# Kernel tuning notes

Hardware: AMD Instinct MI355X
Metric: run time of the kernel (lower is better)

The kernel has to match this reference:

```python
import jax, jax.numpy as jnp
import numpy as np

N = 50000      # nodes
E = 1600000    # edges
IN_DIM = 128
HID = 32
OUT = 32
HEADS = 4
NEG_SLOPE = 0.2  # DGL GATConv default leaky_relu slope


def setup_inputs() -> dict:
    key = jax.random.key(0)
    ks = jax.random.split(key, 16)
    h = jax.random.normal(ks[0], (N, IN_DIM), dtype=jnp.float32)
    src = jax.random.randint(ks[1], (E,), 0, N, dtype=jnp.int32)
    dst = jax.random.randint(ks[2], (E,), 0, N, dtype=jnp.int32)
    s = 0.1
    # layer 1: in_dim -> (HEADS, HID)
    W1 = jax.random.normal(ks[3], (IN_DIM, HEADS * HID), dtype=jnp.float32) * s
    al1 = jax.random.normal(ks[4], (HEADS, HID), dtype=jnp.float32) * s
    ar1 = jax.random.normal(ks[5], (HEADS, HID), dtype=jnp.float32) * s
    b1 = jnp.zeros((HEADS * HID,), dtype=jnp.float32)
    # layer 2: HEADS*HID -> (HEADS, HID)
    W2 = jax.random.normal(ks[6], (HEADS * HID, HEADS * HID), dtype=jnp.float32) * s
    al2 = jax.random.normal(ks[7], (HEADS, HID), dtype=jnp.float32) * s
    ar2 = jax.random.normal(ks[8], (HEADS, HID), dtype=jnp.float32) * s
    b2 = jnp.zeros((HEADS * HID,), dtype=jnp.float32)
    # layer 3: HEADS*HID -> (HEADS, OUT)
    W3 = jax.random.normal(ks[9], (HEADS * HID, HEADS * OUT), dtype=jnp.float32) * s
    al3 = jax.random.normal(ks[10], (HEADS, OUT), dtype=jnp.float32) * s
    ar3 = jax.random.normal(ks[11], (HEADS, OUT), dtype=jnp.float32) * s
    b3 = jnp.zeros((HEADS * OUT,), dtype=jnp.float32)
    return {"h": h, "src": src, "dst": dst,
            "W1": W1, "al1": al1, "ar1": ar1, "b1": b1,
            "W2": W2, "al2": al2, "ar2": ar2, "b2": b2,
            "W3": W3, "al3": al3, "ar3": ar3, "b3": b3}


def gat_layer(h, W, al, ar, b, src, dst):
    """DGL-style GATConv. h:[N,F] -> [N,H,D]."""
    H, D = al.shape
    ft = (h @ W).reshape(-1, H, D)                      # [N,H,D]
    el = jnp.einsum('nhd,hd->nh', ft, al)               # [N,H]
    er = jnp.einsum('nhd,hd->nh', ft, ar)               # [N,H]
    e = jax.nn.leaky_relu(el[src] + er[dst], NEG_SLOPE)  # [E,H]
    # edge softmax grouped by destination node
    m = jax.ops.segment_max(e, dst, num_segments=N)     # [N,H]
    ex = jnp.exp(e - m[dst])
    z = jax.ops.segment_sum(ex, dst, num_segments=N)    # [N,H]
    a = ex / z[dst]                                     # [E,H]
    msg = ft[src] * a[:, :, None]                       # [E,H,D]
    rst = jax.ops.segment_sum(msg, dst, num_segments=N)  # [N,H,D]
    return rst + b.reshape(1, H, D)


def reference(h, src, dst, W1, al1, ar1, b1, W2, al2, ar2, b2, W3, al3, ar3, b3):
    x = gat_layer(h, W1, al1, ar1, b1, src, dst).reshape(N, -1)  # flatten(1)
    x = jax.nn.elu(x)  # dropout is identity at eval
    x = gat_layer(x, W2, al2, ar2, b2, src, dst).reshape(N, -1)
    x = jax.nn.elu(x)
    x = gat_layer(x, W3, al3, ar3, b3, src, dst).mean(axis=1)    # [N,OUT]
    return x
```

## Files before the change

### kernel.cpp

```cpp
#include <hip/hip_runtime.h>
#include <hip/hip_fp16.h>

#define NEG_SLOPE 0.2f
#define LOG2E 1.44269504088896340736f
#define C1   2048
#define BKT  196
#define BSTR 9216

typedef _Float16 half8 __attribute__((ext_vector_type(8)));
typedef float    f32x4 __attribute__((ext_vector_type(4)));

__device__ __forceinline__ unsigned int encf(float f) {
    unsigned int u = __float_as_uint(f);
    return (u & 0x80000000u) ? ~u : (u | 0x80000000u);
}
__device__ __forceinline__ float decf(unsigned int u) {
    return (u & 0x80000000u) ? __uint_as_float(u & 0x7fffffffu)
                             : __uint_as_float(~u);
}

__global__ __launch_bounds__(256) void wprep(const float* __restrict__ W1,
    const float* __restrict__ W2, const float* __restrict__ W3,
    __half* __restrict__ Wt)
{
    __shared__ float tile[32][33];
    const int b = blockIdx.x;
    const float* W = (b < 16) ? W1 : (b < 32) ? W2 : W3;
    __half* out = Wt + (size_t)(b >> 4) * (128 * 128);
    const int tb = b & 15;
    const int k0 = (tb >> 2) * 32;
    const int c0 = (tb & 3) * 32;
    const int t = threadIdx.x;
    const int tx = t & 31, ty = t >> 5;
#pragma unroll
    for (int p = 0; p < 4; ++p)
        tile[p * 8 + ty][tx] = W[(size_t)(k0 + p * 8 + ty) * 128 + c0 + tx];
    __syncthreads();
#pragma unroll
    for (int p = 0; p < 4; ++p) {
        const int c = c0 + p * 8 + ty;
        out[(size_t)c * 128 + k0 + tx] = __float2half(tile[tx][p * 8 + ty]);
    }
}

__global__ __launch_bounds__(256) void gemm_mfma(const float* __restrict__ X,
    const __half* __restrict__ Wt, const float* __restrict__ al,
    const float* __restrict__ ar, __half* __restrict__ C16,
    float* __restrict__ el, float* __restrict__ er,
    unsigned int* __restrict__ maxbuf, int M)
{
    __shared__ __align__(16) char Xs[64 * 256];
    __shared__ __align__(16) char Ws[128 * 256];
    __shared__ unsigned int lmax[8];
    const int t = threadIdx.x;
    const int l = t & 63;
    const int w = t >> 6;
    const int row0 = blockIdx.x * 64;
    if (t < 8) lmax[t] = 0;

    {
        const int r = t >> 2;
        int gr = row0 + r; if (gr >= M) gr = M - 1;
        const float4* s4 = (const float4*)&X[(size_t)gr * 128 + (t & 3) * 32];
        const unsigned swz = ((unsigned)(r & 7)) << 4;
        char* base = Xs + r * 256;
#pragma unroll
        for (int u = 0; u < 4; ++u) {
            float4 a = s4[2 * u], b = s4[2 * u + 1];
            half8 hv;
            hv[0] = (_Float16)a.x; hv[1] = (_Float16)a.y;
            hv[2] = (_Float16)a.z; hv[3] = (_Float16)a.w;
            hv[4] = (_Float16)b.x; hv[5] = (_Float16)b.y;
            hv[6] = (_Float16)b.z; hv[7] = (_Float16)b.w;
            *(half8*)(base + (((t & 3) * 64 + u * 16) ^ swz)) = hv;
        }
    }
    {
        const int c = t >> 1;
        const char* src = (const char*)Wt + (size_t)c * 256 + (t & 1) * 128;
        const unsigned swz = ((unsigned)(c & 7)) << 4;
        char* base = Ws + c * 256;
#pragma unroll
        for (int u = 0; u < 8; ++u) {
            uint4 v = *(const uint4*)(src + u * 16);
            *(uint4*)(base + (((t & 1) * 128 + u * 16) ^ swz)) = v;
        }
    }
    __syncthreads();

    const int wr = w * 16;
    const int rA = l & 15;
    const int kq = l >> 4;

    half8 af[4];
    {
        const int row = wr + rA;
        const unsigned swz = ((unsigned)(row & 7)) << 4;
        const char* base = Xs + row * 256;
#pragma unroll
        for (int kk = 0; kk < 4; ++kk)
            af[kk] = *(const half8*)(base + (((unsigned)(kk * 64 + kq * 16)) ^ swz));
    }
    f32x4 acc[8];
#pragma unroll
    for (int ct = 0; ct < 8; ++ct) { acc[ct][0]=0.f; acc[ct][1]=0.f; acc[ct][2]=0.f; acc[ct][3]=0.f; }
#pragma unroll
    for (int ct = 0; ct < 8; ++ct) {
        const int c = ct * 16 + rA;
        const unsigned swz = ((unsigned)(c & 7)) << 4;
        const char* base = Ws + c * 256;
#pragma unroll
        for (int kk = 0; kk < 4; ++kk) {
            half8 bf = *(const half8*)(base + (((unsigned)(kk * 64 + kq * 16)) ^ swz));
            acc[ct] = __builtin_amdgcn_mfma_f32_16x16x32_f16(af[kk], bf, acc[ct], 0, 0, 0);
        }
    }

    float pl[4][4], pr[4][4];
#pragma unroll
    for (int h = 0; h < 4; ++h)
#pragma unroll
        for (int r = 0; r < 4; ++r) { pl[h][r] = 0.f; pr[h][r] = 0.f; }
#pragma unroll
    for (int ct = 0; ct < 8; ++ct) {
        const int col = ct * 16 + rA;
        const float av = al[col] * LOG2E;
        const float rv = ar[col] * LOG2E;
        const int h = ct >> 1;
#pragma unroll
        for (int r = 0; r < 4; ++r) {
            pl[h][r] += acc[ct][r] * av;
            pr[h][r] += acc[ct][r] * rv;
        }
    }
#pragma unroll
    for (int off = 1; off < 16; off <<= 1) {
#pragma unroll
        for (int h = 0; h < 4; ++h)
#pragma unroll
            for (int r = 0; r < 4; ++r) {
                pl[h][r] += __shfl_xor(pl[h][r], off);
                pr[h][r] += __shfl_xor(pr[h][r], off);
            }
    }
    if (rA == 0) {
#pragma unroll
        for (int r = 0; r < 4; ++r) {
            const int gr = row0 + wr + kq * 4 + r;
            if (gr < M) {
                *(float4*)&el[(size_t)gr * 4] =
                    make_float4(pl[0][r], pl[1][r], pl[2][r], pl[3][r]);
                *(float4*)&er[(size_t)gr * 4] =
                    make_float4(pr[0][r], pr[1][r], pr[2][r], pr[3][r]);
            }
        }
#pragma unroll
        for (int h = 0; h < 4; ++h) {
            float ml = fmaxf(fmaxf(pl[h][0], pl[h][1]), fmaxf(pl[h][2], pl[h][3]));
            float mr = fmaxf(fmaxf(pr[h][0], pr[h][1]), fmaxf(pr[h][2], pr[h][3]));
            atomicMax(&lmax[h], encf(ml));
            atomicMax(&lmax[4 + h], encf(mr));
        }
    }

    {
        char* slice = Xs + wr * 256;
#pragma unroll
        for (int ct = 0; ct < 8; ++ct) {
            const int colb = (ct * 16 + rA) * 2;
#pragma unroll
            for (int r = 0; r < 4; ++r) {
                const int rowL = kq * 4 + r;
                const unsigned swz = ((unsigned)(rowL & 7)) << 4;
                *(__half*)(slice + rowL * 256 + ((unsigned)colb ^ swz)) =
                    __float2half(acc[ct][r]);
            }
        }
        const int rowL = l >> 2;
        const unsigned swz = ((unsigned)(rowL & 7)) << 4;
        const int gr = row0 + wr + rowL;
#pragma unroll
        for (int u = 0; u < 4; ++u) {
            const unsigned bo = (unsigned)((l & 3) * 64 + u * 16);
            uint4 v = *(const uint4*)(slice + rowL * 256 + (bo ^ swz));
            if (gr < M) *(uint4*)&C16[(size_t)gr * 128 + bo / 2] = v;
        }
    }
    __syncthreads();
    if (t < 8) atomicMax(&maxbuf[t], lmax[t]);
}

__global__ __launch_bounds__(256) void p1_bucket(const int* __restrict__ src,
    const int* __restrict__ dst, unsigned int* __restrict__ tmp,
    unsigned int* __restrict__ bcnt, int E_)
{
    __shared__ unsigned int hist[256];
    __shared__ unsigned int sc[256];
    __shared__ unsigned int ebase[256];
    __shared__ unsigned int gbase[256];
    __shared__ unsigned int buf[C1];
    __shared__ unsigned int off[C1];
    const int t  = threadIdx.x;
    const int e0 = blockIdx.x * C1;
    hist[t] = 0;
    __syncthreads();
    int  s_[8], d_[8];
    bool v_[8];
#pragma unroll
    for (int k = 0; k < 2; ++k) {
        int idx = e0 + k * 1024 + t * 4;
        if (idx + 3 < E_) {
            int4 sv = *(const int4*)&src[idx];
            int4 dv = *(const int4*)&dst[idx];
            s_[k*4+0]=sv.x; s_[k*4+1]=sv.y; s_[k*4+2]=sv.z; s_[k*4+3]=sv.w;
            d_[k*4+0]=dv.x; d_[k*4+1]=dv.y; d_[k*4+2]=dv.z; d_[k*4+3]=dv.w;
            v_[k*4+0]=true; v_[k*4+1]=true; v_[k*4+2]=true; v_[k*4+3]=true;
        } else {
            for (int j = 0; j < 4; ++j) {
                int e = idx + j;
                v_[k*4+j] = e < E_;
                s_[k*4+j] = v_[k*4+j] ? src[e] : 0;
                d_[k*4+j] = v_[k*4+j] ? dst[e] : 0;
            }
        }
    }
#pragma unroll
    for (int j = 0; j < 8; ++j) if (v_[j]) atomicAdd(&hist[d_[j] >> 8], 1u);
    __syncthreads();
    const unsigned int cnt_t = hist[t];
    sc[t] = cnt_t;
    __syncthreads();
    for (int o = 1; o < 256; o <<= 1) {
        unsigned int v = (t >= o) ? sc[t - o] : 0;
        __syncthreads();
        sc[t] += v;
        __syncthreads();
    }
    const unsigned int excl = sc[t] - cnt_t;
    ebase[t] = excl;
    gbase[t] = (t < BKT && cnt_t > 0) ? atomicAdd(&bcnt[t], cnt_t) : 0u;
    hist[t] = excl;
    __syncthreads();
#pragma unroll
    for (int j = 0; j < 8; ++j) {
        if (v_[j]) {
            const int b = d_[j] >> 8;
            unsigned int pos  = atomicAdd(&hist[b], 1u);
            unsigned int go   = gbase[b] + (pos - ebase[b]);
            buf[pos] = ((unsigned int)s_[j] << 8) | (unsigned int)(d_[j] & 255);
            off[pos] = (go < BSTR) ? ((unsigned int)b * BSTR + go) : 0xFFFFFFFFu;
        }
    }
    __syncthreads();
    const int total = min(C1, E_ - e0);
    for (int i = t; i < total; i += 256) {
        unsigned int u = off[i];
        if (u != 0xFFFFFFFFu) tmp[u] = buf[i];
    }
}

__global__ __launch_bounds__(256) void scanB(const unsigned int* __restrict__ bcnt,
    unsigned int* __restrict__ bbase, unsigned int* __restrict__ maxinit, int E_)
{
    __shared__ unsigned int sc[256];
    const int t = threadIdx.x;
    const unsigned int v = (t < BKT) ? bcnt[t] : 0;
    sc[t] = v;
    __syncthreads();
    for (int off = 1; off < 256; off <<= 1) {
        unsigned int u = (t >= off) ? sc[t - off] : 0;
        __syncthreads();
        sc[t] += u;
        __syncthreads();
    }
    if (t < BKT) bbase[t] = sc[t] - v;
    if (t == BKT) bbase[t] = (unsigned int)E_;
    if (t < 24) maxinit[t] = 0;
}

__global__ __launch_bounds__(512) void p2_scatter(const unsigned int* __restrict__ tmp,
    const unsigned int* __restrict__ bcnt, const unsigned int* __restrict__ bbase,
    int* __restrict__ rowptr, int* __restrict__ esrc_s, int Nn)
{
    __shared__ unsigned int hist[256], sc[256], cur[256];
    __shared__ unsigned int ent[BSTR];
    const int t = threadIdx.x;
    const int b = blockIdx.x;
    const unsigned int cnt  = min(bcnt[b], (unsigned int)BSTR);
    const unsigned int base = bbase[b];
    if (t < 256) hist[t] = 0;
    __syncthreads();
    for (unsigned int i = t; i < cnt; i += 512) {
        unsigned int e = tmp[(size_t)b * BSTR + i];
        ent[i] = e;
        atomicAdd(&hist[e & 255u], 1u);
    }
    __syncthreads();
    unsigned int c_t = 0;
    if (t < 256) { c_t = hist[t]; sc[t] = c_t; }
    __syncthreads();
    for (int off = 1; off < 256; off <<= 1) {
        unsigned int u = (t < 256 && t >= off) ? sc[t - off] : 0;
        __syncthreads();
        if (t < 256) sc[t] += u;
        __syncthreads();
    }
    if (t < 256) {
        const unsigned int excl = sc[t] - c_t;
        cur[t] = base + excl;
        const int n = (b << 8) + t;
        if (n <= Nn) rowptr[n] = (int)(base + excl);
    }
    __syncthreads();
    for (unsigned int i = t; i < cnt; i += 512) {
        unsigned int e = ent[i];
        unsigned int p = atomicAdd(&cur[e & 255u], 1u);
        esrc_s[p] = (int)(e >> 8);
    }
}

template <int MODE>
__global__ __launch_bounds__(256) void attn_agg(
    const __half* __restrict__ ft, const float* __restrict__ el,
    const float* __restrict__ er, const int* __restrict__ rowptr,
    const int* __restrict__ esrc, const float* __restrict__ bias,
    const unsigned int* __restrict__ mbuf, float* __restrict__ out, int Nn)
{
    const int t = threadIdx.x;
    const int l = t & 63;
    const int n = blockIdx.x * 4 + (t >> 6);
    if (n >= Nn) return;
    const int g    = l >> 4;
    const int q    = l & 15;
    const int head = q >> 2;

    const int start = rowptr[n];
    const int end   = rowptr[n + 1];
    const bool any  = end > start;

    const float er_h = er[(size_t)n * 4 + head];
    const float msum = decf(mbuf[head]) + decf(mbuf[4 + head]);
    const float mh   = msum > 0.f ? msum : NEG_SLOPE * msum;

    const char* __restrict__ ftb = (const char*)ft;
    const char* __restrict__ elb = (const char*)el;
    const unsigned qo = (unsigned)q << 4;
    const unsigned ho = (unsigned)head << 2;

    float acc[8];
#pragma unroll
    for (int j = 0; j < 8; ++j) acc[j] = 0.f;
    float z = 0.f;

    const int c0   = start & ~3;
    const int last = end - 1;
    const int span = end - start;

    int  sA = 0, sB = 0, sC = 0;
    uint4 fA = make_uint4(0,0,0,0), fB;
    float eA = 0.f, eB;

    if (any) {
        int e0i = min(max(c0 + g, start), last);
        int e1i = min(max(c0 + 4 + g, start), last);
        sA = esrc[e0i];
        sB = esrc[e1i];
        fA = *(const uint4*)(ftb + ((unsigned)sA << 8) + qo);
        eA = *(const float*)(elb + ((unsigned)sA << 4) + ho);
    }

#pragma unroll 2
    for (int c = c0; c < end; c += 4) {
        sC = esrc[min(c + 8 + g, last)];
        fB = *(const uint4*)(ftb + ((unsigned)sB << 8) + qo);
        eB = *(const float*)(elb + ((unsigned)sB << 4) + ho);
        {
            const int e = c + g;
            float x = eA + er_h;
            x = fmaxf(x, NEG_SLOPE * x);
            float ex = __builtin_amdgcn_exp2f(x - mh);
            ex = ((unsigned)(e - start) < (unsigned)span) ? ex : 0.f;
            z += ex;
            const half8 hv = __builtin_bit_cast(half8, fA);
            acc[0] += (float)hv[0] * ex;
            acc[1] += (float)hv[1] * ex;
            acc[2] += (float)hv[2] * ex;
            acc[3] += (float)hv[3] * ex;
            acc[4] += (float)hv[4] * ex;
            acc[5] += (float)hv[5] * ex;
            acc[6] += (float)hv[6] * ex;
            acc[7] += (float)hv[7] * ex;
        }
        sA = sB; sB = sC; fA = fB; eA = eB;
    }

#pragma unroll
    for (int j = 0; j < 8; ++j) {
        acc[j] += __shfl_xor(acc[j], 16);
        acc[j] += __shfl_xor(acc[j], 32);
    }
    z += __shfl_xor(z, 16);
    z += __shfl_xor(z, 32);

    const float inv = any ? 1.f / z : 0.f;

    if (MODE == 0) {
        if (l < 32) {
            float r0, r1, r2, r3;
            if (l < 16) { r0 = acc[0]; r1 = acc[1]; r2 = acc[2]; r3 = acc[3]; }
            else        { r0 = acc[4]; r1 = acc[5]; r2 = acc[6]; r3 = acc[7]; }
            const int f0 = 8 * q + 4 * (l >> 4);
            const float4 b4 = *(const float4*)&bias[f0];
            float vx = r0 * inv + b4.x;
            float vy = r1 * inv + b4.y;
            float vz = r2 * inv + b4.z;
            float vw = r3 * inv + b4.w;
            vx = vx > 0.f ? vx : __expf(vx) - 1.f;
            vy = vy > 0.f ? vy : __expf(vy) - 1.f;
            vz = vz > 0.f ? vz : __expf(vz) - 1.f;
            vw = vw > 0.f ? vw : __expf(vw) - 1.f;
            *(float4*)&out[(size_t)n * 128 + f0] = make_float4(vx, vy, vz, vw);
        }
    } else {
        float v[8];
        const float4 ba = *(const float4*)&bias[8 * q];
        const float4 bb = *(const float4*)&bias[8 * q + 4];
        v[0] = acc[0] * inv + ba.x; v[1] = acc[1] * inv + ba.y;
        v[2] = acc[2] * inv + ba.z; v[3] = acc[3] * inv + ba.w;
        v[4] = acc[4] * inv + bb.x; v[5] = acc[5] * inv + bb.y;
        v[6] = acc[6] * inv + bb.z; v[7] = acc[7] * inv + bb.w;
#pragma unroll
        for (int j = 0; j < 8; ++j) {
            v[j] += __shfl_xor(v[j], 4);
            v[j] += __shfl_xor(v[j], 8);
        }
        if (l < 4) {
            *(float4*)&out[(size_t)n * 32 + 8 * q] =
                make_float4(0.25f * v[0], 0.25f * v[1], 0.25f * v[2], 0.25f * v[3]);
            *(float4*)&out[(size_t)n * 32 + 8 * q + 4] =
                make_float4(0.25f * v[4], 0.25f * v[5], 0.25f * v[6], 0.25f * v[7]);
        }
    }
}

extern "C" void kernel_launch(void* const* d_in, const int* in_sizes, int n_in,
                              void* d_out, int out_size, void* d_ws, size_t ws_size,
                              hipStream_t stream)
{
    const float* h   = (const float*)d_in[0];
    const int*   src = (const int*)d_in[1];
    const int*   dst = (const int*)d_in[2];
    const float* W1  = (const float*)d_in[3];
    const float* al1 = (const float*)d_in[4];
    const float* ar1 = (const float*)d_in[5];
    const float* b1  = (const float*)d_in[6];
    const float* W2  = (const float*)d_in[7];
    const float* al2 = (const float*)d_in[8];
    const float* ar2 = (const float*)d_in[9];
    const float* b2  = (const float*)d_in[10];
    const float* W3  = (const float*)d_in[11];
    const float* al3 = (const float*)d_in[12];
    const float* ar3 = (const float*)d_in[13];
    const float* b3  = (const float*)d_in[14];

    const int N = in_sizes[0] / 128;
    const int E = in_sizes[1];

    char* p = (char*)d_ws;
    auto alloc = [&](size_t bytes) {
        void* r = (void*)p;
        p += (bytes + 255) & ~(size_t)255;
        return r;
    };
    __half* ft    = (__half*)alloc((size_t)N * 128 * 4);
    float* xA     = (float*)alloc((size_t)N * 128 * 4);
    float* elbuf  = (float*)alloc((size_t)N * 4 * 4);
    float* erbuf  = (float*)alloc((size_t)N * 4 * 4);
    int*   rowptr = (int*)alloc((size_t)(N + 1) * 4);
    int*   esrc_s = (int*)alloc((size_t)E * 4);
    unsigned int* bcnt   = (unsigned int*)alloc((size_t)BKT * 4);
    unsigned int* bbase  = (unsigned int*)alloc((size_t)(BKT + 1) * 4);
    unsigned int* maxbuf = (unsigned int*)alloc(24 * 4);
    __half* Wt    = (__half*)alloc((size_t)3 * 128 * 128 * 2);

    unsigned int* tmp = (unsigned int*)ft;

    const int NG4 = (N + 3) / 4;
    const int MG  = (N + 63) / 64;
    const int G1  = (E + C1 - 1) / C1;

    hipMemsetAsync(bcnt, 0, (size_t)BKT * 4, stream);
    wprep<<<48, 256, 0, stream>>>(W1, W2, W3, Wt);
    p1_bucket<<<G1, 256, 0, stream>>>(src, dst, tmp, bcnt, E);
    scanB<<<1, 256, 0, stream>>>(bcnt, bbase, maxbuf, E);
    p2_scatter<<<BKT, 512, 0, stream>>>(tmp, bcnt, bbase, rowptr, esrc_s, N);

    gemm_mfma<<<MG, 256, 0, stream>>>(h, Wt, al1, ar1, ft, elbuf, erbuf, maxbuf, N);
    attn_agg<0><<<NG4, 256, 0, stream>>>(ft, elbuf, erbuf, rowptr, esrc_s, b1, maxbuf, xA, N);

    gemm_mfma<<<MG, 256, 0, stream>>>(xA, Wt + 128 * 128, al2, ar2, ft, elbuf, erbuf, maxbuf + 8, N);
    attn_agg<0><<<NG4, 256, 0, stream>>>(ft, elbuf, erbuf, rowptr, esrc_s, b2, maxbuf + 8, xA, N);

    gemm_mfma<<<MG, 256, 0, stream>>>(xA, Wt + 2 * 128 * 128, al3, ar3, ft, elbuf, erbuf, maxbuf + 16, N);
    attn_agg<1><<<NG4, 256, 0, stream>>>(ft, elbuf, erbuf, rowptr, esrc_s, b3, maxbuf + 16,
                                         (float*)d_out, N);
}
```

Baseline: 382.2 us.

## Merge preprocessing kernels and overlap CSR scatter with first-layer GEMM

Weight transpose and edge bucketing now run as one launch (fusedA), split by block index. The bucket scan moves into each scatter block, and the scatter runs alongside the first-layer GEMM in a second fused launch (fusedB), which removes the scanB kernel and lets independent work share the GPU. The temp bucket buffer moves from ft to xA so it does not collide with the GEMM output, and the memset now also clears the max buffers. The cost is that each scatter block repeats the 256-entry scan, scatter blocks now use 256 threads instead of 512, and the fused kernels reserve the larger shared-memory footprint for every block.

```diff
diff --git a/kernel.cpp b/kernel.cpp
--- a/kernel.cpp
+++ b/kernel.cpp
@@ -19,12 +19,12 @@
                              : __uint_as_float(~u);
 }
 
-__global__ __launch_bounds__(256) void wprep(const float* __restrict__ W1,
-    const float* __restrict__ W2, const float* __restrict__ W3,
-    __half* __restrict__ Wt)
-{
-    __shared__ float tile[32][33];
-    const int b = blockIdx.x;
+
+__device__ __forceinline__ void wprep_body(char* SM, int b,
+    const float* __restrict__ W1, const float* __restrict__ W2,
+    const float* __restrict__ W3, __half* __restrict__ Wt)
+{
+    float (*tile)[33] = (float(*)[33])SM;
     const float* W = (b < 16) ? W1 : (b < 32) ? W2 : W3;
     __half* out = Wt + (size_t)(b >> 4) * (128 * 128);
     const int tb = b & 15;
@@ -43,165 +43,18 @@
     }
 }
 
-__global__ __launch_bounds__(256) void gemm_mfma(const float* __restrict__ X,
-    const __half* __restrict__ Wt, const float* __restrict__ al,
-    const float* __restrict__ ar, __half* __restrict__ C16,
-    float* __restrict__ el, float* __restrict__ er,
-    unsigned int* __restrict__ maxbuf, int M)
-{
-    __shared__ __align__(16) char Xs[64 * 256];
-    __shared__ __align__(16) char Ws[128 * 256];
-    __shared__ unsigned int lmax[8];
-    const int t = threadIdx.x;
-    const int l = t & 63;
-    const int w = t >> 6;
-    const int row0 = blockIdx.x * 64;
-    if (t < 8) lmax[t] = 0;
-
-    {
-        const int r = t >> 2;
-        int gr = row0 + r; if (gr >= M) gr = M - 1;
-        const float4* s4 = (const float4*)&X[(size_t)gr * 128 + (t & 3) * 32];
-        const unsigned swz = ((unsigned)(r & 7)) << 4;
-        char* base = Xs + r * 256;
-#pragma unroll
-        for (int u = 0; u < 4; ++u) {
-            float4 a = s4[2 * u], b = s4[2 * u + 1];
-            half8 hv;
-            hv[0] = (_Float16)a.x; hv[1] = (_Float16)a.y;
-            hv[2] = (_Float16)a.z; hv[3] = (_Float16)a.w;
-            hv[4] = (_Float16)b.x; hv[5] = (_Float16)b.y;
-            hv[6] = (_Float16)b.z; hv[7] = (_Float16)b.w;
-            *(half8*)(base + (((t & 3) * 64 + u * 16) ^ swz)) = hv;
-        }
-    }
-    {
-        const int c = t >> 1;
-        const char* src = (const char*)Wt + (size_t)c * 256 + (t & 1) * 128;
-        const unsigned swz = ((unsigned)(c & 7)) << 4;
-        char* base = Ws + c * 256;
-#pragma unroll
-        for (int u = 0; u < 8; ++u) {
-            uint4 v = *(const uint4*)(src + u * 16);
-            *(uint4*)(base + (((t & 1) * 128 + u * 16) ^ swz)) = v;
-        }
-    }
-    __syncthreads();
-
-    const int wr = w * 16;
-    const int rA = l & 15;
-    const int kq = l >> 4;
-
-    half8 af[4];
-    {
-        const int row = wr + rA;
-        const unsigned swz = ((unsigned)(row & 7)) << 4;
-        const char* base = Xs + row * 256;
-#pragma unroll
-        for (int kk = 0; kk < 4; ++kk)
-            af[kk] = *(const half8*)(base + (((unsigned)(kk * 64 + kq * 16)) ^ swz));
-    }
-    f32x4 acc[8];
-#pragma unroll
-    for (int ct = 0; ct < 8; ++ct) { acc[ct][0]=0.f; acc[ct][1]=0.f; acc[ct][2]=0.f; acc[ct][3]=0.f; }
-#pragma unroll
-    for (int ct = 0; ct < 8; ++ct) {
-        const int c = ct * 16 + rA;
-        const unsigned swz = ((unsigned)(c & 7)) << 4;
-        const char* base = Ws + c * 256;
-#pragma unroll
-        for (int kk = 0; kk < 4; ++kk) {
-            half8 bf = *(const half8*)(base + (((unsigned)(kk * 64 + kq * 16)) ^ swz));
-            acc[ct] = __builtin_amdgcn_mfma_f32_16x16x32_f16(af[kk], bf, acc[ct], 0, 0, 0);
-        }
-    }
-
-    float pl[4][4], pr[4][4];
-#pragma unroll
-    for (int h = 0; h < 4; ++h)
-#pragma unroll
-        for (int r = 0; r < 4; ++r) { pl[h][r] = 0.f; pr[h][r] = 0.f; }
-#pragma unroll
-    for (int ct = 0; ct < 8; ++ct) {
-        const int col = ct * 16 + rA;
-        const float av = al[col] * LOG2E;
-        const float rv = ar[col] * LOG2E;
-        const int h = ct >> 1;
-#pragma unroll
-        for (int r = 0; r < 4; ++r) {
-            pl[h][r] += acc[ct][r] * av;
-            pr[h][r] += acc[ct][r] * rv;
-        }
-    }
-#pragma unroll
-    for (int off = 1; off < 16; off <<= 1) {
-#pragma unroll
-        for (int h = 0; h < 4; ++h)
-#pragma unroll
-            for (int r = 0; r < 4; ++r) {
-                pl[h][r] += __shfl_xor(pl[h][r], off);
-                pr[h][r] += __shfl_xor(pr[h][r], off);
-            }
-    }
-    if (rA == 0) {
-#pragma unroll
-        for (int r = 0; r < 4; ++r) {
-            const int gr = row0 + wr + kq * 4 + r;
-            if (gr < M) {
-                *(float4*)&el[(size_t)gr * 4] =
-                    make_float4(pl[0][r], pl[1][r], pl[2][r], pl[3][r]);
-                *(float4*)&er[(size_t)gr * 4] =
-                    make_float4(pr[0][r], pr[1][r], pr[2][r], pr[3][r]);
-            }
-        }
-#pragma unroll
-        for (int h = 0; h < 4; ++h) {
-            float ml = fmaxf(fmaxf(pl[h][0], pl[h][1]), fmaxf(pl[h][2], pl[h][3]));
-            float mr = fmaxf(fmaxf(pr[h][0], pr[h][1]), fmaxf(pr[h][2], pr[h][3]));
-            atomicMax(&lmax[h], encf(ml));
-            atomicMax(&lmax[4 + h], encf(mr));
-        }
-    }
-
-    {
-        char* slice = Xs + wr * 256;
-#pragma unroll
-        for (int ct = 0; ct < 8; ++ct) {
-            const int colb = (ct * 16 + rA) * 2;
-#pragma unroll
-            for (int r = 0; r < 4; ++r) {
-                const int rowL = kq * 4 + r;
-                const unsigned swz = ((unsigned)(rowL & 7)) << 4;
-                *(__half*)(slice + rowL * 256 + ((unsigned)colb ^ swz)) =
-                    __float2half(acc[ct][r]);
-            }
-        }
-        const int rowL = l >> 2;
-        const unsigned swz = ((unsigned)(rowL & 7)) << 4;
-        const int gr = row0 + wr + rowL;
-#pragma unroll
-        for (int u = 0; u < 4; ++u) {
-            const unsigned bo = (unsigned)((l & 3) * 64 + u * 16);
-            uint4 v = *(const uint4*)(slice + rowL * 256 + (bo ^ swz));
-            if (gr < M) *(uint4*)&C16[(size_t)gr * 128 + bo / 2] = v;
-        }
-    }
-    __syncthreads();
-    if (t < 8) atomicMax(&maxbuf[t], lmax[t]);
-}
-
-__global__ __launch_bounds__(256) void p1_bucket(const int* __restrict__ src,
-    const int* __restrict__ dst, unsigned int* __restrict__ tmp,
-    unsigned int* __restrict__ bcnt, int E_)
-{
-    __shared__ unsigned int hist[256];
-    __shared__ unsigned int sc[256];
-    __shared__ unsigned int ebase[256];
-    __shared__ unsigned int gbase[256];
-    __shared__ unsigned int buf[C1];
-    __shared__ unsigned int off[C1];
+__device__ __forceinline__ void p1_body(char* SM, int blk,
+    const int* __restrict__ src, const int* __restrict__ dst,
+    unsigned int* __restrict__ tmp, unsigned int* __restrict__ bcnt, int E_)
+{
+    unsigned int* hist  = (unsigned int*)SM;
+    unsigned int* sc    = hist + 256;
+    unsigned int* ebase = sc + 256;
+    unsigned int* gbase = ebase + 256;
+    unsigned int* buf   = gbase + 256;
+    unsigned int* off   = buf + C1;
     const int t  = threadIdx.x;
-    const int e0 = blockIdx.x * C1;
+    const int e0 = blk * C1;
     hist[t] = 0;
     __syncthreads();
     int  s_[8], d_[8];
@@ -259,64 +112,238 @@
     }
 }
 
-__global__ __launch_bounds__(256) void scanB(const unsigned int* __restrict__ bcnt,
-    unsigned int* __restrict__ bbase, unsigned int* __restrict__ maxinit, int E_)
-{
-    __shared__ unsigned int sc[256];
+__device__ __forceinline__ void p2_body(char* SM, int b,
+    const unsigned int* __restrict__ tmp, const unsigned int* __restrict__ bcnt,
+    int* __restrict__ rowptr, int* __restrict__ esrc_s, int Nn)
+{
+    unsigned int* ent  = (unsigned int*)SM;
+    unsigned int* hist = ent + BSTR;
+    unsigned int* sc   = hist + 256;
+    unsigned int* cur  = sc + 256;
     const int t = threadIdx.x;
-    const unsigned int v = (t < BKT) ? bcnt[t] : 0;
-    sc[t] = v;
-    __syncthreads();
-    for (int off = 1; off < 256; off <<= 1) {
-        unsigned int u = (t >= off) ? sc[t - off] : 0;
+    const unsigned int vt = (t < BKT) ? bcnt[t] : 0;
+    sc[t] = vt;
+    __syncthreads();
+    for (int o = 1; o < 256; o <<= 1) {
+        unsigned int u = (t >= o) ? sc[t - o] : 0;
         __syncthreads();
         sc[t] += u;
         __syncthreads();
     }
-    if (t < BKT) bbase[t] = sc[t] - v;
-    if (t == BKT) bbase[t] = (unsigned int)E_;
-    if (t < 24) maxinit[t] = 0;
-}
-
-__global__ __launch_bounds__(512) void p2_scatter(const unsigned int* __restrict__ tmp,
-    const unsigned int* __restrict__ bcnt, const unsigned int* __restrict__ bbase,
-    int* __restrict__ rowptr, int* __restrict__ esrc_s, int Nn)
-{
-    __shared__ unsigned int hist[256], sc[256], cur[256];
-    __shared__ unsigned int ent[BSTR];
-    const int t = threadIdx.x;
-    const int b = blockIdx.x;
+    const unsigned int base = (b > 0) ? sc[b - 1] : 0;
     const unsigned int cnt  = min(bcnt[b], (unsigned int)BSTR);
-    const unsigned int base = bbase[b];
-    if (t < 256) hist[t] = 0;
-    __syncthreads();
-    for (unsigned int i = t; i < cnt; i += 512) {
+    __syncthreads();
+    hist[t] = 0;
+    __syncthreads();
+    for (unsigned int i = t; i < cnt; i += 256) {
         unsigned int e = tmp[(size_t)b * BSTR + i];
         ent[i] = e;
         atomicAdd(&hist[e & 255u], 1u);
     }
     __syncthreads();
-    unsigned int c_t = 0;
-    if (t < 256) { c_t = hist[t]; sc[t] = c_t; }
-    __syncthreads();
-    for (int off = 1; off < 256; off <<= 1) {
-        unsigned int u = (t < 256 && t >= off) ? sc[t - off] : 0;
+    const unsigned int c_t = hist[t];
+    sc[t] = c_t;
+    __syncthreads();
+    for (int o = 1; o < 256; o <<= 1) {
+        unsigned int u = (t >= o) ? sc[t - o] : 0;
         __syncthreads();
-        if (t < 256) sc[t] += u;
+        sc[t] += u;
         __syncthreads();
     }
-    if (t < 256) {
-        const unsigned int excl = sc[t] - c_t;
-        cur[t] = base + excl;
-        const int n = (b << 8) + t;
-        if (n <= Nn) rowptr[n] = (int)(base + excl);
-    }
-    __syncthreads();
-    for (unsigned int i = t; i < cnt; i += 512) {
+    const unsigned int excl = sc[t] - c_t;
+    cur[t] = base + excl;
+    const int n = (b << 8) + t;
+    if (n <= Nn) rowptr[n] = (int)(base + excl);
+    __syncthreads();
+    for (unsigned int i = t; i < cnt; i += 256) {
         unsigned int e = ent[i];
         unsigned int p = atomicAdd(&cur[e & 255u], 1u);
         esrc_s[p] = (int)(e >> 8);
     }
+}
+
+__device__ __forceinline__ void gemm_body(char* SMEM, unsigned int* lmax,
+    int row0, const float* __restrict__ X, const __half* __restrict__ Wt,
+    const float* __restrict__ al, const float* __restrict__ ar,
+    __half* __restrict__ C16, float* __restrict__ el, float* __restrict__ er,
+    unsigned int* __restrict__ maxbuf, int M)
+{
+    char* Xs = SMEM;
+    char* Ws = SMEM + 64 * 256;
+    const int t = threadIdx.x;
+    const int l = t & 63;
+    const int w = t >> 6;
+    if (t < 8) lmax[t] = 0;
+
+    {
+        const int r = t >> 2;
+        int gr = row0 + r; if (gr >= M) gr = M - 1;
+        const float4* s4 = (const float4*)&X[(size_t)gr * 128 + (t & 3) * 32];
+        const unsigned swz = ((unsigned)(r & 7)) << 4;
+        char* base = Xs + r * 256;
+#pragma unroll
+        for (int u = 0; u < 4; ++u) {
+            float4 a = s4[2 * u], b = s4[2 * u + 1];
+            half8 hv;
+            hv[0] = (_Float16)a.x; hv[1] = (_Float16)a.y;
+            hv[2] = (_Float16)a.z; hv[3] = (_Float16)a.w;
+            hv[4] = (_Float16)b.x; hv[5] = (_Float16)b.y;
+            hv[6] = (_Float16)b.z; hv[7] = (_Float16)b.w;
+            *(half8*)(base + (((t & 3) * 64 + u * 16) ^ swz)) = hv;
+        }
+    }
+    {
+        const int c = t >> 1;
+        const char* src = (const char*)Wt + (size_t)c * 256 + (t & 1) * 128;
+        const unsigned swz = ((unsigned)(c & 7)) << 4;
+        char* base = Ws + c * 256;
+#pragma unroll
+        for (int u = 0; u < 8; ++u) {
+            uint4 v = *(const uint4*)(src + u * 16);
+            *(uint4*)(base + (((t & 1) * 128 + u * 16) ^ swz)) = v;
+        }
+    }
+    __syncthreads();
+
+    const int wr = w * 16;
+    const int rA = l & 15;
+    const int kq = l >> 4;
+
+    half8 af[4];
+    {
+        const int row = wr + rA;
+        const unsigned swz = ((unsigned)(row & 7)) << 4;
+        const char* base = Xs + row * 256;
+#pragma unroll
+        for (int kk = 0; kk < 4; ++kk)
+            af[kk] = *(const half8*)(base + (((unsigned)(kk * 64 + kq * 16)) ^ swz));
+    }
+    f32x4 acc[8];
+#pragma unroll
+    for (int ct = 0; ct < 8; ++ct) { acc[ct][0]=0.f; acc[ct][1]=0.f; acc[ct][2]=0.f; acc[ct][3]=0.f; }
+#pragma unroll
+    for (int ct = 0; ct < 8; ++ct) {
+        const int c = ct * 16 + rA;
+        const unsigned swz = ((unsigned)(c & 7)) << 4;
+        const char* base = Ws + c * 256;
+#pragma unroll
+        for (int kk = 0; kk < 4; ++kk) {
+            half8 bf = *(const half8*)(base + (((unsigned)(kk * 64 + kq * 16)) ^ swz));
+            acc[ct] = __builtin_amdgcn_mfma_f32_16x16x32_f16(af[kk], bf, acc[ct], 0, 0, 0);
+        }
+    }
+
+    float pl[4][4], pr[4][4];
+#pragma unroll
+    for (int h = 0; h < 4; ++h)
+#pragma unroll
+        for (int r = 0; r < 4; ++r) { pl[h][r] = 0.f; pr[h][r] = 0.f; }
+#pragma unroll
+    for (int ct = 0; ct < 8; ++ct) {
+        const int col = ct * 16 + rA;
+        const float av = al[col] * LOG2E;
+        const float rv = ar[col] * LOG2E;
+        const int h = ct >> 1;
+#pragma unroll
+        for (int r = 0; r < 4; ++r) {
+            pl[h][r] += acc[ct][r] * av;
+            pr[h][r] += acc[ct][r] * rv;
+        }
+    }
+#pragma unroll
+    for (int off = 1; off < 16; off <<= 1) {
+#pragma unroll
+        for (int h = 0; h < 4; ++h)
+#pragma unroll
+            for (int r = 0; r < 4; ++r) {
+                pl[h][r] += __shfl_xor(pl[h][r], off);
+                pr[h][r] += __shfl_xor(pr[h][r], off);
+            }
+    }
+    if (rA == 0) {
+#pragma unroll
+        for (int r = 0; r < 4; ++r) {
+            const int gr = row0 + wr + kq * 4 + r;
+            if (gr < M) {
+                *(float4*)&el[(size_t)gr * 4] =
+                    make_float4(pl[0][r], pl[1][r], pl[2][r], pl[3][r]);
+                *(float4*)&er[(size_t)gr * 4] =
+                    make_float4(pr[0][r], pr[1][r], pr[2][r], pr[3][r]);
+            }
+        }
+#pragma unroll
+        for (int h = 0; h < 4; ++h) {
+            float ml = fmaxf(fmaxf(pl[h][0], pl[h][1]), fmaxf(pl[h][2], pl[h][3]));
+            float mr = fmaxf(fmaxf(pr[h][0], pr[h][1]), fmaxf(pr[h][2], pr[h][3]));
+            atomicMax(&lmax[h], encf(ml));
+            atomicMax(&lmax[4 + h], encf(mr));
+        }
+    }
+
+    {
+        char* slice = Xs + wr * 256;
+#pragma unroll
+        for (int ct = 0; ct < 8; ++ct) {
+            const int colb = (ct * 16 + rA) * 2;
+#pragma unroll
+            for (int r = 0; r < 4; ++r) {
+                const int rowL = kq * 4 + r;
+                const unsigned swz = ((unsigned)(rowL & 7)) << 4;
+                *(__half*)(slice + rowL * 256 + ((unsigned)colb ^ swz)) =
+                    __float2half(acc[ct][r]);
+            }
+        }
+        const int rowL = l >> 2;
+        const unsigned swz = ((unsigned)(rowL & 7)) << 4;
+        const int gr = row0 + wr + rowL;
+#pragma unroll
+        for (int u = 0; u < 4; ++u) {
+            const unsigned bo = (unsigned)((l & 3) * 64 + u * 16);
+            uint4 v = *(const uint4*)(slice + rowL * 256 + (bo ^ swz));
+            if (gr < M) *(uint4*)&C16[(size_t)gr * 128 + bo / 2] = v;
+        }
+    }
+    __syncthreads();
+    if (t < 8) atomicMax(&maxbuf[t], lmax[t]);
+}
+
+
+__global__ __launch_bounds__(256) void fusedA(const float* __restrict__ W1,
+    const float* __restrict__ W2, const float* __restrict__ W3,
+    __half* __restrict__ Wt, const int* __restrict__ src,
+    const int* __restrict__ dst, unsigned int* __restrict__ tmp,
+    unsigned int* __restrict__ bcnt, int E_)
+{
+    __shared__ __align__(16) char SM[20480];
+    if (blockIdx.x < 48) wprep_body(SM, blockIdx.x, W1, W2, W3, Wt);
+    else                 p1_body(SM, blockIdx.x - 48, src, dst, tmp, bcnt, E_);
+}
+
+__global__ __launch_bounds__(256) void fusedB(const float* __restrict__ X,
+    const __half* __restrict__ Wt, const float* __restrict__ al,
+    const float* __restrict__ ar, __half* __restrict__ C16,
+    float* __restrict__ el, float* __restrict__ er,
+    unsigned int* __restrict__ maxbuf, int M, int MG,
+    const unsigned int* __restrict__ tmp, const unsigned int* __restrict__ bcnt,
+    int* __restrict__ rowptr, int* __restrict__ esrc_s)
+{
+    __shared__ __align__(16) char SMEM[49152];
+    __shared__ unsigned int lmax[8];
+    if ((int)blockIdx.x < MG)
+        gemm_body(SMEM, lmax, blockIdx.x * 64, X, Wt, al, ar, C16, el, er, maxbuf, M);
+    else
+        p2_body(SMEM, blockIdx.x - MG, tmp, bcnt, rowptr, esrc_s, M);
+}
+
+__global__ __launch_bounds__(256) void gemm_mfma(const float* __restrict__ X,
+    const __half* __restrict__ Wt, const float* __restrict__ al,
+    const float* __restrict__ ar, __half* __restrict__ C16,
+    float* __restrict__ el, float* __restrict__ er,
+    unsigned int* __restrict__ maxbuf, int M)
+{
+    __shared__ __align__(16) char SMEM[49152];
+    __shared__ unsigned int lmax[8];
+    gemm_body(SMEM, lmax, blockIdx.x * 64, X, Wt, al, ar, C16, el, er, maxbuf, M);
 }
 
 template <int MODE>
@@ -472,30 +499,26 @@
         p += (bytes + 255) & ~(size_t)255;
         return r;
     };
-    __half* ft    = (__half*)alloc((size_t)N * 128 * 4);
+    __half* ft    = (__half*)alloc((size_t)N * 128 * 2);
     float* xA     = (float*)alloc((size_t)N * 128 * 4);
     float* elbuf  = (float*)alloc((size_t)N * 4 * 4);
     float* erbuf  = (float*)alloc((size_t)N * 4 * 4);
     int*   rowptr = (int*)alloc((size_t)(N + 1) * 4);
     int*   esrc_s = (int*)alloc((size_t)E * 4);
-    unsigned int* bcnt   = (unsigned int*)alloc((size_t)BKT * 4);
-    unsigned int* bbase  = (unsigned int*)alloc((size_t)(BKT + 1) * 4);
-    unsigned int* maxbuf = (unsigned int*)alloc(24 * 4);
+    unsigned int* bcnt   = (unsigned int*)alloc((256 + 24) * 4);
+    unsigned int* maxbuf = bcnt + 256;
     __half* Wt    = (__half*)alloc((size_t)3 * 128 * 128 * 2);
 
-    unsigned int* tmp = (unsigned int*)ft;
+    unsigned int* tmp = (unsigned int*)xA;
 
     const int NG4 = (N + 3) / 4;
     const int MG  = (N + 63) / 64;
     const int G1  = (E + C1 - 1) / C1;
 
-    hipMemsetAsync(bcnt, 0, (size_t)BKT * 4, stream);
-    wprep<<<48, 256, 0, stream>>>(W1, W2, W3, Wt);
-    p1_bucket<<<G1, 256, 0, stream>>>(src, dst, tmp, bcnt, E);
-    scanB<<<1, 256, 0, stream>>>(bcnt, bbase, maxbuf, E);
-    p2_scatter<<<BKT, 512, 0, stream>>>(tmp, bcnt, bbase, rowptr, esrc_s, N);
-
-    gemm_mfma<<<MG, 256, 0, stream>>>(h, Wt, al1, ar1, ft, elbuf, erbuf, maxbuf, N);
+    hipMemsetAsync(bcnt, 0, (256 + 24) * 4, stream);
+    fusedA<<<48 + G1, 256, 0, stream>>>(W1, W2, W3, Wt, src, dst, tmp, bcnt, E);
+    fusedB<<<MG + BKT, 256, 0, stream>>>(h, Wt, al1, ar1, ft, elbuf, erbuf,
+                                         maxbuf, N, MG, tmp, bcnt, rowptr, esrc_s);
     attn_agg<0><<<NG4, 256, 0, stream>>>(ft, elbuf, erbuf, rowptr, esrc_s, b1, maxbuf, xA, N);
 
     gemm_mfma<<<MG, 256, 0, stream>>>(xA, Wt + 128 * 128, al2, ar2, ft, elbuf, erbuf, maxbuf + 8, N);
```

Result: faster. 374.2 us (-2.1%).
